# Kernel tuning notes

Measured on AMD Instinct MI355X. Metric: run time of the kernel, lower is better.

## Reference

```python
import jax, jax.numpy as jnp
import numpy as np

B, H, HKV, S, D = 2, 32, 8, 2048, 64
SCALE = 0.125  # 1/sqrt(D)
EPS = 1e-9     # kernel divides by (l + 1e-9)


def setup_inputs() -> dict:
    key = jax.random.key(0)
    kq, kk, kv = jax.random.split(key, 3)
    Q = jax.random.normal(kq, (B, H, S, D), dtype=jnp.float32)
    K = jax.random.normal(kk, (B, HKV, S, D), dtype=jnp.float32)
    V = jax.random.normal(kv, (B, HKV, S, D), dtype=jnp.float32)
    return {"Q": Q, "K": K, "V": V}


def reference(Q, K, V):
    # Grouped-query attention with KV-head sharing, non-causal, full softmax.
    b, h, s, d = Q.shape
    hkv = K.shape[1]
    g = h // hkv  # query heads per kv head; h = kvh*g + gi (contiguous groups)
    Qg = Q.reshape(b, hkv, g, s, d)
    # scores: [b, hkv, g, s_q, s_k]
    scores = jnp.einsum("bkgsd,bktd->bkgst", Qg, K) * SCALE
    m = jnp.max(scores, axis=-1, keepdims=True)
    p = jnp.exp(scores - m)
    l = jnp.sum(p, axis=-1, keepdims=True)  # [b,hkv,g,s,1]
    out = jnp.einsum("bkgst,bktd->bkgsd", p, V) / (l + EPS)
    return out.reshape(b, h, s, d)
```

## Files before the change

kernel.cpp:

```cpp
#include <hip/hip_runtime.h>

#define NB 2
#define NH 32
#define NKV 8
#define SEQ 2048
#define DH 64
#define TQ 256
#define TK 64

typedef _Float16 f16x4 __attribute__((ext_vector_type(4)));
typedef _Float16 f16x8 __attribute__((ext_vector_type(8)));
typedef float f32x4 __attribute__((ext_vector_type(4)));

#define MFMA(A, B, C) __builtin_amdgcn_mfma_f32_16x16x32_f16(A, B, C, 0, 0, 0)

__device__ __forceinline__ int swz(int row, int hcol) {
  return (row << 6) + ((((hcol >> 3) ^ (row & 7)) << 3) | (hcol & 7));
}

__global__ __launch_bounds__(256, 2) void gqa_fused(
    const float* __restrict__ Qg, const float* __restrict__ Kg,
    const float* __restrict__ Vg, float* __restrict__ Og) {
  __shared__ _Float16 Kt[2][TK * DH];
  __shared__ _Float16 Vt[2][DH * TK];
  __shared__ _Float16 Pt[TQ * TK];

  const int tid  = threadIdx.x;
  const int wave = tid >> 6;
  const int lane = tid & 63;
  const int quad = lane >> 4;
  const int l16  = lane & 15;

  const int qt  = blockIdx.x;
  const int hq  = blockIdx.y;
  const int b   = blockIdx.z;
  const int hkv = hq >> 2;

  const float* Qb = Qg + (((size_t)b * NH + hq) * SEQ + (size_t)qt * TQ) * DH;
  const float* Kb = Kg + ((size_t)b * NKV + hkv) * (size_t)SEQ * DH;
  const float* Vb = Vg + ((size_t)b * NKV + hkv) * (size_t)SEQ * DH;
  float* Ob       = Og + (((size_t)b * NH + hq) * SEQ + (size_t)qt * TQ) * DH;

  const float qscale = 0.125f * 1.44269504088896341f;

  f16x8 aQ[4][2];
#pragma unroll
  for (int sl = 0; sl < 4; ++sl) {
    const float* qp = Qb + (size_t)(wave * 64 + sl * 16 + l16) * DH + quad * 8;
#pragma unroll
    for (int c = 0; c < 2; ++c) {
      const float4 f0 = *reinterpret_cast<const float4*>(qp + c * 32);
      const float4 f1 = *reinterpret_cast<const float4*>(qp + c * 32 + 4);
      union { f16x8 v; _Float16 e[8]; } u;
      u.e[0] = (_Float16)(f0.x * qscale);
      u.e[1] = (_Float16)(f0.y * qscale);
      u.e[2] = (_Float16)(f0.z * qscale);
      u.e[3] = (_Float16)(f0.w * qscale);
      u.e[4] = (_Float16)(f1.x * qscale);
      u.e[5] = (_Float16)(f1.y * qscale);
      u.e[6] = (_Float16)(f1.z * qscale);
      u.e[7] = (_Float16)(f1.w * qscale);
      aQ[sl][c] = u.v;
    }
  }

  f32x4 o[4][4], ol[4];
#pragma unroll
  for (int sl = 0; sl < 4; ++sl) {
    ol[sl] = (f32x4){0.f, 0.f, 0.f, 0.f};
#pragma unroll
    for (int n = 0; n < 4; ++n) o[sl][n] = (f32x4){0.f, 0.f, 0.f, 0.f};
  }
  const f16x8 ones = {(_Float16)1.f, (_Float16)1.f, (_Float16)1.f, (_Float16)1.f,
                      (_Float16)1.f, (_Float16)1.f, (_Float16)1.f, (_Float16)1.f};

  const int kkey = tid >> 3;
  const int kd8  = (tid & 7) << 3;
  float4 kpre[2][2];
  float vpre[2][8];
  auto load_tile = [&](int kt) {
#pragma unroll
    for (int it = 0; it < 2; ++it) {
      const float* kp = Kb + (size_t)(kt + it * 32 + kkey) * DH + kd8;
      kpre[it][0] = *reinterpret_cast<const float4*>(kp);
      kpre[it][1] = *reinterpret_cast<const float4*>(kp + 4);
    }
#pragma unroll
    for (int ao = 0; ao < 2; ++ao) {
      const int a = wave + 4 * ao;
      const float* vp = Vb + (size_t)(kt + 2 * a) * DH + lane;
#pragma unroll
      for (int t = 0; t < 4; ++t) {
        vpre[ao][t]     = vp[(size_t)(16 * t) * DH];
        vpre[ao][t + 4] = vp[(size_t)(16 * t + 1) * DH];
      }
    }
  };

  auto stage_tile = [&](int buf) {
#pragma unroll
    for (int it = 0; it < 2; ++it) {
      union { f16x8 v; _Float16 e[8]; } u;
      u.e[0] = (_Float16)kpre[it][0].x;
      u.e[1] = (_Float16)kpre[it][0].y;
      u.e[2] = (_Float16)kpre[it][0].z;
      u.e[3] = (_Float16)kpre[it][0].w;
      u.e[4] = (_Float16)kpre[it][1].x;
      u.e[5] = (_Float16)kpre[it][1].y;
      u.e[6] = (_Float16)kpre[it][1].z;
      u.e[7] = (_Float16)kpre[it][1].w;
      *reinterpret_cast<f16x8*>(&Kt[buf][swz(it * 32 + kkey, kd8)]) = u.v;
    }
#pragma unroll
    for (int ao = 0; ao < 2; ++ao) {
      union { f16x8 v; _Float16 e[8]; } u;
#pragma unroll
      for (int j = 0; j < 8; ++j) u.e[j] = (_Float16)vpre[ao][j];
      *reinterpret_cast<f16x8*>(&Vt[buf][swz(lane, 8 * (wave + 4 * ao))]) = u.v;
    }
  };

  load_tile(0);
  stage_tile(0);
  __syncthreads();

  for (int kt = 0; kt < SEQ; kt += TK) {
    const int cur  = (kt >> 6) & 1;
    const bool more = (kt + TK) < SEQ;
    if (more) load_tile(kt + TK);

    f16x8 bK[4][2];
#pragma unroll
    for (int n = 0; n < 4; ++n)
#pragma unroll
      for (int c = 0; c < 2; ++c)
        bK[n][c] = *reinterpret_cast<const f16x8*>(
            &Kt[cur][swz(n * 16 + l16, c * 32 + quad * 8)]);

    f32x4 s[4][4];
#pragma unroll
    for (int sl = 0; sl < 4; ++sl)
#pragma unroll
      for (int n = 0; n < 4; ++n) {
        f32x4 acc = (f32x4){0.f, 0.f, 0.f, 0.f};
        acc = MFMA(aQ[sl][0], bK[n][0], acc);
        acc = MFMA(aQ[sl][1], bK[n][1], acc);
        s[sl][n] = acc;
      }

#pragma unroll
    for (int sl = 0; sl < 4; ++sl) {
      const int prow = wave * 64 + sl * 16 + quad * 4;
#pragma unroll
      for (int r = 0; r < 4; ++r) {
        union { f16x4 v; _Float16 e[4]; } u;
#pragma unroll
        for (int n = 0; n < 4; ++n)
          u.e[n] = (_Float16)__builtin_amdgcn_exp2f(s[sl][n][r]);
        *reinterpret_cast<f16x4*>(&Pt[swz(prow + r, l16 << 2)]) = u.v;
      }
    }
    __asm__ volatile("s_waitcnt lgkmcnt(0)" ::: "memory");

    f16x8 aP[4][2], bV[4][2];
#pragma unroll
    for (int sl = 0; sl < 4; ++sl)
#pragma unroll
      for (int c = 0; c < 2; ++c)
        aP[sl][c] = *reinterpret_cast<const f16x8*>(
            &Pt[swz(wave * 64 + sl * 16 + l16, c * 32 + quad * 8)]);
#pragma unroll
    for (int n = 0; n < 4; ++n)
#pragma unroll
      for (int c = 0; c < 2; ++c)
        bV[n][c] = *reinterpret_cast<const f16x8*>(
            &Vt[cur][swz(n * 16 + l16, c * 32 + quad * 8)]);

#pragma unroll
    for (int sl = 0; sl < 4; ++sl) {
      ol[sl] = MFMA(aP[sl][0], ones, ol[sl]);
      ol[sl] = MFMA(aP[sl][1], ones, ol[sl]);
#pragma unroll
      for (int n = 0; n < 4; ++n) {
        o[sl][n] = MFMA(aP[sl][0], bV[n][0], o[sl][n]);
        o[sl][n] = MFMA(aP[sl][1], bV[n][1], o[sl][n]);
      }
    }

    if (more) stage_tile(cur ^ 1);
    __syncthreads();
  }

#pragma unroll
  for (int sl = 0; sl < 4; ++sl)
#pragma unroll
    for (int r = 0; r < 4; ++r) {
      const float inv = 1.f / (ol[sl][r] + 1e-9f);
      const size_t row = (size_t)(wave * 64 + sl * 16 + quad * 4 + r);
#pragma unroll
      for (int n = 0; n < 4; ++n)
        Ob[row * DH + n * 16 + l16] = o[sl][n][r] * inv;
    }
}

extern "C" void kernel_launch(void* const* d_in, const int* in_sizes, int n_in,
                              void* d_out, int out_size, void* d_ws, size_t ws_size,
                              hipStream_t stream) {
  const float* Q = (const float*)d_in[0];
  const float* K = (const float*)d_in[1];
  const float* V = (const float*)d_in[2];
  float* O = (float*)d_out;
  dim3 grid(SEQ / TQ, NH, NB);
  gqa_fused<<<grid, 256, 0, stream>>>(Q, K, V, O);
}
```

Baseline: 169.3 us.

## Accumulate softmax row sums in registers instead of ones-MFMA, interleave score and exp

Replaces the MFMA against a ones vector, which computed the row sums of P, with per-lane fp32 accumulation of the exp values. The partial sums are reduced across the 16 lanes with xor shuffles once at the end. The score computation is fused per 16-row slice with the exp and P store, and the next K/V global prefetch moves into the middle of that loop. The launch-bounds occupancy hint of 2 is dropped. The goal is fewer MFMA instructions and lower register pressure, at the cost of extra VALU adds and a possible change in occupancy.

```diff
diff --git a/kernel.cpp b/kernel.cpp
--- a/kernel.cpp
+++ b/kernel.cpp
@@ -18,7 +18,7 @@
   return (row << 6) + ((((hcol >> 3) ^ (row & 7)) << 3) | (hcol & 7));
 }
 
-__global__ __launch_bounds__(256, 2) void gqa_fused(
+__global__ __launch_bounds__(256) void gqa_fused(
     const float* __restrict__ Qg, const float* __restrict__ Kg,
     const float* __restrict__ Vg, float* __restrict__ Og) {
   __shared__ _Float16 Kt[2][TK * DH];
@@ -64,15 +64,13 @@
     }
   }
 
-  f32x4 o[4][4], ol[4];
+  f32x4 o[4][4], lp[4];
 #pragma unroll
   for (int sl = 0; sl < 4; ++sl) {
-    ol[sl] = (f32x4){0.f, 0.f, 0.f, 0.f};
+    lp[sl] = (f32x4){0.f, 0.f, 0.f, 0.f};
 #pragma unroll
     for (int n = 0; n < 4; ++n) o[sl][n] = (f32x4){0.f, 0.f, 0.f, 0.f};
   }
-  const f16x8 ones = {(_Float16)1.f, (_Float16)1.f, (_Float16)1.f, (_Float16)1.f,
-                      (_Float16)1.f, (_Float16)1.f, (_Float16)1.f, (_Float16)1.f};
 
   const int kkey = tid >> 3;
   const int kd8  = (tid & 7) << 3;
@@ -125,9 +123,8 @@
   __syncthreads();
 
   for (int kt = 0; kt < SEQ; kt += TK) {
-    const int cur  = (kt >> 6) & 1;
+    const int cur   = (kt >> 6) & 1;
     const bool more = (kt + TK) < SEQ;
-    if (more) load_tile(kt + TK);
 
     f16x8 bK[4][2];
 #pragma unroll
@@ -137,28 +134,31 @@
         bK[n][c] = *reinterpret_cast<const f16x8*>(
             &Kt[cur][swz(n * 16 + l16, c * 32 + quad * 8)]);
 
-    f32x4 s[4][4];
-#pragma unroll
-    for (int sl = 0; sl < 4; ++sl)
+#pragma unroll
+    for (int sl = 0; sl < 4; ++sl) {
+      f32x4 s[4];
 #pragma unroll
       for (int n = 0; n < 4; ++n) {
         f32x4 acc = (f32x4){0.f, 0.f, 0.f, 0.f};
         acc = MFMA(aQ[sl][0], bK[n][0], acc);
         acc = MFMA(aQ[sl][1], bK[n][1], acc);
-        s[sl][n] = acc;
-      }
-
-#pragma unroll
-    for (int sl = 0; sl < 4; ++sl) {
+        s[n] = acc;
+      }
       const int prow = wave * 64 + sl * 16 + quad * 4;
 #pragma unroll
       for (int r = 0; r < 4; ++r) {
         union { f16x4 v; _Float16 e[4]; } u;
-#pragma unroll
-        for (int n = 0; n < 4; ++n)
-          u.e[n] = (_Float16)__builtin_amdgcn_exp2f(s[sl][n][r]);
+        float lacc = 0.f;
+#pragma unroll
+        for (int n = 0; n < 4; ++n) {
+          const float e = __builtin_amdgcn_exp2f(s[n][r]);
+          lacc += e;
+          u.e[n] = (_Float16)e;
+        }
+        lp[sl][r] += lacc;
         *reinterpret_cast<f16x4*>(&Pt[swz(prow + r, l16 << 2)]) = u.v;
       }
+      if (sl == 1 && more) load_tile(kt + TK);
     }
     __asm__ volatile("s_waitcnt lgkmcnt(0)" ::: "memory");
 
@@ -177,15 +177,12 @@
             &Vt[cur][swz(n * 16 + l16, c * 32 + quad * 8)]);
 
 #pragma unroll
-    for (int sl = 0; sl < 4; ++sl) {
-      ol[sl] = MFMA(aP[sl][0], ones, ol[sl]);
-      ol[sl] = MFMA(aP[sl][1], ones, ol[sl]);
+    for (int sl = 0; sl < 4; ++sl)
 #pragma unroll
       for (int n = 0; n < 4; ++n) {
         o[sl][n] = MFMA(aP[sl][0], bV[n][0], o[sl][n]);
         o[sl][n] = MFMA(aP[sl][1], bV[n][1], o[sl][n]);
       }
-    }
 
     if (more) stage_tile(cur ^ 1);
     __syncthreads();
@@ -195,7 +192,12 @@
   for (int sl = 0; sl < 4; ++sl)
 #pragma unroll
     for (int r = 0; r < 4; ++r) {
-      const float inv = 1.f / (ol[sl][r] + 1e-9f);
+      float sum = lp[sl][r];
+      sum += __shfl_xor(sum, 1);
+      sum += __shfl_xor(sum, 2);
+      sum += __shfl_xor(sum, 4);
+      sum += __shfl_xor(sum, 8);
+      const float inv = 1.f / (sum + 1e-9f);
       const size_t row = (size_t)(wave * 64 + sl * 16 + quad * 4 + r);
 #pragma unroll
       for (int n = 0; n < 4; ++n)
```

Measured after the change: 196.1 us. 15.8% more time.
